# Optimization experiments

Measured on AMD Instinct MI355X. Metric: run time of the kernel, lower is better.

The kernel has to match this reference:

```python
import jax, jax.numpy as jnp
import numpy as np


def setup_inputs() -> dict:
    key = jax.random.key(0)
    rain_hr = jax.random.normal(key, (16, 8, 1, 512, 512), dtype=jnp.float32)
    return {"rain_hr": rain_hr}


def reference(rain_hr):
    B, T, C, H, W = rain_hr.shape
    rain_mean = rain_hr.mean(axis=1)              # [B, C, H, W]

    fft = jnp.fft.fft2(rain_mean)                 # complex [B, C, H, W]
    power = jnp.abs(fft) ** 2                     # [B, C, H, W]

    # Integer radius map (torch: sqrt(...).long() truncates toward zero)
    ch, cw = H // 2, W // 2
    y = jnp.arange(H, dtype=jnp.float32) - ch
    x = jnp.arange(W, dtype=jnp.float32) - cw
    radius = jnp.sqrt(x[None, :] ** 2 + y[:, None] ** 2).astype(jnp.int32)  # [H, W]

    max_radius = min(H, W) // 2

    # power[..., mask].mean() == sum over (B, C, pixels at radius r) / (B*C*count_r)
    power_hw = power.sum(axis=(0, 1))             # [H, W]
    flat_r = radius.ravel()
    # out-of-range radii (>= max_radius) are dropped by segment_sum
    seg_sum = jax.ops.segment_sum(power_hw.ravel(), flat_r, num_segments=max_radius)
    counts = jax.ops.segment_sum(jnp.ones((H * W,), jnp.float32), flat_r, num_segments=max_radius)

    cnt = counts[1:]                               # radii 1 .. max_radius-1
    denom = jnp.maximum(cnt, 1.0) * (B * C)
    gen_spectrum = jnp.where(cnt > 0, seg_sum[1:] / denom, 0.0)

    k = jnp.arange(1, max_radius, dtype=jnp.float32)
    ref = k ** (-5.0 / 3.0)
    ref = ref / (ref.sum() + 1e-8)

    gen_norm = gen_spectrum / (gen_spectrum.sum() + 1e-8)
    loss = jnp.mean((gen_norm - ref) ** 2)
    return loss
```

## Files before the change

### kernel.cpp

```cpp
#include <hip/hip_runtime.h>
#include <math.h>

#define N 512
#define PLANE ((size_t)N * N)
#define NEG2PI (-6.28318530717958647692f)

__device__ inline void dft8(float (&xr)[8], float (&xi)[8]) {
    const float S = 0.70710678118654752440f;
    float t0r = xr[0] + xr[4], t0i = xi[0] + xi[4];
    float t4r = xr[0] - xr[4], t4i = xi[0] - xi[4];
    float t1r = xr[1] + xr[5], t1i = xi[1] + xi[5];
    float t5r = xr[1] - xr[5], t5i = xi[1] - xi[5];
    float t2r = xr[2] + xr[6], t2i = xi[2] + xi[6];
    float t6r = xr[2] - xr[6], t6i = xi[2] - xi[6];
    float t3r = xr[3] + xr[7], t3i = xi[3] + xi[7];
    float t7r = xr[3] - xr[7], t7i = xi[3] - xi[7];
    float o1r = S * (t5r + t5i), o1i = S * (t5i - t5r);
    float o2r = t6i,             o2i = -t6r;
    float o3r = S * (t7i - t7r), o3i = -S * (t7r + t7i);
    float p0r = t0r + t2r, p0i = t0i + t2i;
    float p1r = t1r + t3r, p1i = t1i + t3i;
    float q0r = t0r - t2r, q0i = t0i - t2i;
    float q1r = t1i - t3i, q1i = -(t1r - t3r);
    xr[0] = p0r + p1r; xi[0] = p0i + p1i;
    xr[4] = p0r - p1r; xi[4] = p0i - p1i;
    xr[2] = q0r + q1r; xi[2] = q0i + q1i;
    xr[6] = q0r - q1r; xi[6] = q0i - q1i;
    float r0r = t4r + o2r, r0i = t4i + o2i;
    float r1r = o1r + o3r, r1i = o1i + o3i;
    float u0r = t4r - o2r, u0i = t4i - o2i;
    float u1r = o1i - o3i, u1i = -(o1r - o3r);
    xr[1] = r0r + r1r; xi[1] = r0i + r1i;
    xr[5] = r0r - r1r; xi[5] = r0i - r1i;
    xr[3] = u0r + u1r; xi[3] = u0i + u1i;
    xr[7] = u0r - u1r; xi[7] = u0i - u1i;
}

__device__ inline void twiddle_apply(float (&xr)[8], float (&xi)[8], float ang1) {
    float ts, tc;
    __sincosf(ang1, &ts, &tc);
    float wr = tc, wi = ts;
    #pragma unroll
    for (int k = 1; k < 8; ++k) {
        float nr = xr[k] * wr - xi[k] * wi;
        float ni = xr[k] * wi + xi[k] * wr;
        xr[k] = nr; xi[k] = ni;
        float w2r = wr * tc - wi * ts;
        float w2i = wr * ts + wi * tc;
        wr = w2r; wi = w2i;
    }
}

__device__ inline void fft512_wave(float (&xr)[8], float (&xi)[8],
                                   float* sre, float* sim, const int l) {
    dft8(xr, xi);
    twiddle_apply(xr, xi, (NEG2PI / 512.0f) * (float)l);
    const int w0 = l + (l >> 3);
    #pragma unroll
    for (int k = 0; k < 8; ++k) { sre[72 * k + w0] = xr[k]; sim[72 * k + w0] = xi[k]; }
    const int i2 = l & 7;
    const int rbase = 72 * (l >> 3) + i2;
    #pragma unroll
    for (int q = 0; q < 8; ++q) { xr[q] = sre[rbase + 9 * q]; xi[q] = sim[rbase + 9 * q]; }
    dft8(xr, xi);
    twiddle_apply(xr, xi, (NEG2PI / 64.0f) * (float)i2);
    #pragma unroll
    for (int k = 0; k < 8; ++k) { sre[rbase + 9 * k] = xr[k]; sim[rbase + 9 * k] = xi[k]; }
    const int r3 = 9 * l;
    #pragma unroll
    for (int q = 0; q < 8; ++q) { xr[q] = sre[r3 + q]; xi[q] = sim[r3 + q]; }
    dft8(xr, xi);
}

__global__ __launch_bounds__(256, 4) void kern_rowfft(const float* __restrict__ in,
                                                      float2* __restrict__ ws) {
    __shared__ float sRe[4][576];
    __shared__ float sIm[4][576];
    const int wv = threadIdx.x >> 6;
    const int l  = threadIdx.x & 63;
    const int y  = blockIdx.x * 4 + wv;
    const int j  = blockIdx.y;
    const float* baseA = in + ((size_t)j * 8) * PLANE + (size_t)y * N;
    const float* baseB = in + ((size_t)(j + 8) * 8) * PLANE + (size_t)y * N;
    float* re = sRe[wv];
    float* im = sIm[wv];
    #pragma unroll
    for (int c0 = 0; c0 < 2; ++c0) {
        const int c = l + 64 * c0;
        float4 sa = make_float4(0.f, 0.f, 0.f, 0.f);
        float4 sb = make_float4(0.f, 0.f, 0.f, 0.f);
        #pragma unroll
        for (int tt = 0; tt < 8; ++tt) {
            float4 a = *(const float4*)(baseA + tt * PLANE + 4 * c);
            float4 b = *(const float4*)(baseB + tt * PLANE + 4 * c);
            sa.x += a.x; sa.y += a.y; sa.z += a.z; sa.w += a.w;
            sb.x += b.x; sb.y += b.y; sb.z += b.z; sb.w += b.w;
        }
        const int i0 = 4 * c;
        const int p0 = i0 + (i0 >> 3);
        re[p0 + 0] = sa.x * 0.125f; re[p0 + 1] = sa.y * 0.125f;
        re[p0 + 2] = sa.z * 0.125f; re[p0 + 3] = sa.w * 0.125f;
        im[p0 + 0] = sb.x * 0.125f; im[p0 + 1] = sb.y * 0.125f;
        im[p0 + 2] = sb.z * 0.125f; im[p0 + 3] = sb.w * 0.125f;
    }
    float xr[8], xi[8];
    #pragma unroll
    for (int q = 0; q < 8; ++q) {
        const int p = l + (l >> 3) + 72 * q;
        xr[q] = re[p]; xi[q] = im[p];
    }
    fft512_wave(xr, xi, re, im, l);
    float2* wp = ws + ((size_t)j << 18) + ((size_t)y << 9);
    #pragma unroll
    for (int k = 0; k < 8; ++k) {
        wp[64 * k + 8 * (l & 7) + (l >> 3)] = make_float2(xr[k], xi[k]);
    }
}

__global__ __launch_bounds__(512, 4) void kern_colfft(const float2* __restrict__ ws,
                                                      float* __restrict__ gseg,
                                                      float* __restrict__ gcnt) {
    __shared__ float sA[8 * 576];
    __shared__ float sB[8 * 576];
    __shared__ float lseg[256];
    __shared__ float lcnt[256];
    const int w   = threadIdx.x >> 6;
    const int l   = threadIdx.x & 63;
    const int fx0 = blockIdx.x * 8;
    const int j   = blockIdx.y;
    if (threadIdx.x < 256) { lseg[threadIdx.x] = 0.f; lcnt[threadIdx.x] = 0.f; }
    const float2* base = ws + ((size_t)j << 18) + fx0;
    #pragma unroll
    for (int i = 0; i < 8; ++i) {
        const int y = (w << 6) + (i << 3) + (l >> 3);
        const int f = l & 7;
        float2 v = base[((size_t)y << 9) + f];
        sA[y * 9 + f] = v.x;
        sB[y * 9 + f] = v.y;
    }
    __syncthreads();
    float xr[8], xi[8];
    #pragma unroll
    for (int q = 0; q < 8; ++q) {
        const int y = l + (q << 6);
        xr[q] = sA[y * 9 + w];
        xi[q] = sB[y * 9 + w];
    }
    __syncthreads();
    fft512_wave(xr, xi, sA + w * 576, sB + w * 576, l);
    const int dx  = fx0 + w - 256;
    const int dx2 = dx * dx;
    #pragma unroll
    for (int k = 0; k < 8; ++k) {
        const int fy = 64 * k + 8 * (l & 7) + (l >> 3);
        const int dy = fy - 256;
        const int d2 = dx2 + dy * dy;
        int r = (int)sqrtf((float)d2);
        if ((r + 1) * (r + 1) <= d2) r++;
        else if (r * r > d2) r--;
        if (r >= 1 && r < 256) {
            atomicAdd(&lseg[r], xr[k] * xr[k] + xi[k] * xi[k]);
            if (j == 0) atomicAdd(&lcnt[r], 1.0f);
        }
    }
    __syncthreads();
    const int t = threadIdx.x;
    if (t < 256) {
        if (lseg[t] != 0.f) atomicAdd(&gseg[j * 256 + t], lseg[t]);
    } else if (j == 0) {
        if (lcnt[t - 256] != 0.f) atomicAdd(&gcnt[t - 256], lcnt[t - 256]);
    }
}

__global__ __launch_bounds__(256) void kern_loss(const float* __restrict__ gseg,
                                                 const float* __restrict__ gcnt,
                                                 float* __restrict__ out) {
    __shared__ float red[256];
    const int t = threadIdx.x;
    float gen = 0.f, refv = 0.f;
    if (t >= 1) {
        float s = 0.f;
        #pragma unroll
        for (int j = 0; j < 8; ++j) s += gseg[j * 256 + t];
        float c = gcnt[t];
        gen  = (c > 0.f) ? s / (fmaxf(c, 1.f) * 16.0f) : 0.f;
        refv = powf((float)t, -5.0f / 3.0f);
    }
    red[t] = gen; __syncthreads();
    for (int off = 128; off > 0; off >>= 1) {
        if (t < off) red[t] += red[t + off];
        __syncthreads();
    }
    const float sgen = red[0]; __syncthreads();
    red[t] = refv; __syncthreads();
    for (int off = 128; off > 0; off >>= 1) {
        if (t < off) red[t] += red[t + off];
        __syncthreads();
    }
    const float sref = red[0]; __syncthreads();
    const float gn = gen  / (sgen + 1e-8f);
    const float rn = refv / (sref + 1e-8f);
    red[t] = (gn - rn) * (gn - rn); __syncthreads();
    for (int off = 128; off > 0; off >>= 1) {
        if (t < off) red[t] += red[t + off];
        __syncthreads();
    }
    if (t == 0) out[0] = red[0] / 255.0f;
}

extern "C" void kernel_launch(void* const* d_in, const int* in_sizes, int n_in,
                              void* d_out, int out_size, void* d_ws, size_t ws_size,
                              hipStream_t stream) {
    const float* in = (const float*)d_in[0];
    float2* planes = (float2*)d_ws;
    float* bins = (float*)((char*)d_ws + (size_t)8 * N * N * sizeof(float2));
    float* gseg = bins;
    float* gcnt = bins + 8 * 256;
    hipMemsetAsync(bins, 0, (8 * 256 + 256) * sizeof(float), stream);
    kern_rowfft<<<dim3(128, 8), 256, 0, stream>>>(in, planes);
    kern_colfft<<<dim3(64, 8), 512, 0, stream>>>(planes, gseg, gcnt);
    kern_loss<<<1, 256, 0, stream>>>(gseg, gcnt, (float*)d_out);
}
```

Measured before the change: 216.8 us.

## Fold bin zeroing into row FFT, interleave block order, batch loads

```diff
diff --git a/kernel.cpp b/kernel.cpp
--- a/kernel.cpp
+++ b/kernel.cpp
@@ -37,8 +37,7 @@
 }
 
 __device__ inline void twiddle_apply(float (&xr)[8], float (&xi)[8], float ang1) {
-    float ts, tc;
-    __sincosf(ang1, &ts, &tc);
+    float ts = __sinf(ang1), tc = __cosf(ang1);
     float wr = tc, wi = ts;
     #pragma unroll
     for (int k = 1; k < 8; ++k) {
@@ -73,13 +72,20 @@
 }
 
 __global__ __launch_bounds__(256, 4) void kern_rowfft(const float* __restrict__ in,
-                                                      float2* __restrict__ ws) {
+                                                      float2* __restrict__ ws,
+                                                      float* __restrict__ bins) {
     __shared__ float sRe[4][576];
     __shared__ float sIm[4][576];
-    const int wv = threadIdx.x >> 6;
-    const int l  = threadIdx.x & 63;
-    const int y  = blockIdx.x * 4 + wv;
-    const int j  = blockIdx.y;
+    const int b   = blockIdx.x;
+    const int j   = b & 7;
+    const int sub = b >> 3;
+    const int wv  = threadIdx.x >> 6;
+    const int l   = threadIdx.x & 63;
+    const int y   = sub * 4 + wv;
+    if (b == 0) {
+        #pragma unroll
+        for (int i = 0; i < 9; ++i) bins[i * 256 + threadIdx.x] = 0.f;
+    }
     const float* baseA = in + ((size_t)j * 8) * PLANE + (size_t)y * N;
     const float* baseB = in + ((size_t)(j + 8) * 8) * PLANE + (size_t)y * N;
     float* re = sRe[wv];
@@ -87,15 +93,20 @@
     #pragma unroll
     for (int c0 = 0; c0 < 2; ++c0) {
         const int c = l + 64 * c0;
-        float4 sa = make_float4(0.f, 0.f, 0.f, 0.f);
-        float4 sb = make_float4(0.f, 0.f, 0.f, 0.f);
-        #pragma unroll
-        for (int tt = 0; tt < 8; ++tt) {
-            float4 a = *(const float4*)(baseA + tt * PLANE + 4 * c);
-            float4 b = *(const float4*)(baseB + tt * PLANE + 4 * c);
-            sa.x += a.x; sa.y += a.y; sa.z += a.z; sa.w += a.w;
-            sb.x += b.x; sb.y += b.y; sb.z += b.z; sb.w += b.w;
-        }
+        float4 va[8], vb[8];
+        #pragma unroll
+        for (int tt = 0; tt < 8; ++tt) va[tt] = *(const float4*)(baseA + tt * PLANE + 4 * c);
+        #pragma unroll
+        for (int tt = 0; tt < 8; ++tt) vb[tt] = *(const float4*)(baseB + tt * PLANE + 4 * c);
+        float4 sa, sb;
+        sa.x = ((va[0].x + va[1].x) + (va[2].x + va[3].x)) + ((va[4].x + va[5].x) + (va[6].x + va[7].x));
+        sa.y = ((va[0].y + va[1].y) + (va[2].y + va[3].y)) + ((va[4].y + va[5].y) + (va[6].y + va[7].y));
+        sa.z = ((va[0].z + va[1].z) + (va[2].z + va[3].z)) + ((va[4].z + va[5].z) + (va[6].z + va[7].z));
+        sa.w = ((va[0].w + va[1].w) + (va[2].w + va[3].w)) + ((va[4].w + va[5].w) + (va[6].w + va[7].w));
+        sb.x = ((vb[0].x + vb[1].x) + (vb[2].x + vb[3].x)) + ((vb[4].x + vb[5].x) + (vb[6].x + vb[7].x));
+        sb.y = ((vb[0].y + vb[1].y) + (vb[2].y + vb[3].y)) + ((vb[4].y + vb[5].y) + (vb[6].y + vb[7].y));
+        sb.z = ((vb[0].z + vb[1].z) + (vb[2].z + vb[3].z)) + ((vb[4].z + vb[5].z) + (vb[6].z + vb[7].z));
+        sb.w = ((vb[0].w + vb[1].w) + (vb[2].w + vb[3].w)) + ((vb[4].w + vb[5].w) + (vb[6].w + vb[7].w));
         const int i0 = 4 * c;
         const int p0 = i0 + (i0 >> 3);
         re[p0 + 0] = sa.x * 0.125f; re[p0 + 1] = sa.y * 0.125f;
@@ -124,11 +135,14 @@
     __shared__ float sB[8 * 576];
     __shared__ float lseg[256];
     __shared__ float lcnt[256];
-    const int w   = threadIdx.x >> 6;
-    const int l   = threadIdx.x & 63;
-    const int fx0 = blockIdx.x * 8;
-    const int j   = blockIdx.y;
-    if (threadIdx.x < 256) { lseg[threadIdx.x] = 0.f; lcnt[threadIdx.x] = 0.f; }
+    const int b   = blockIdx.x;
+    const int j   = b & 7;
+    const int sub = b >> 3;
+    const int fx0 = sub * 8;
+    const int t   = threadIdx.x;
+    const int w   = t >> 6;
+    const int l   = t & 63;
+    if (t < 256) { lseg[t] = 0.f; lcnt[t] = 0.f; }
     const float2* base = ws + ((size_t)j << 18) + fx0;
     #pragma unroll
     for (int i = 0; i < 8; ++i) {
@@ -164,7 +178,6 @@
         }
     }
     __syncthreads();
-    const int t = threadIdx.x;
     if (t < 256) {
         if (lseg[t] != 0.f) atomicAdd(&gseg[j * 256 + t], lseg[t]);
     } else if (j == 0) {
@@ -181,10 +194,10 @@
     if (t >= 1) {
         float s = 0.f;
         #pragma unroll
-        for (int j = 0; j < 8; ++j) s += gseg[j * 256 + t];
+        for (int jj = 0; jj < 8; ++jj) s += gseg[jj * 256 + t];
         float c = gcnt[t];
         gen  = (c > 0.f) ? s / (fmaxf(c, 1.f) * 16.0f) : 0.f;
-        refv = powf((float)t, -5.0f / 3.0f);
+        refv = exp2f(-1.66666666667f * log2f((float)t));
     }
     red[t] = gen; __syncthreads();
     for (int off = 128; off > 0; off >>= 1) {
@@ -216,8 +229,7 @@
     float* bins = (float*)((char*)d_ws + (size_t)8 * N * N * sizeof(float2));
     float* gseg = bins;
     float* gcnt = bins + 8 * 256;
-    hipMemsetAsync(bins, 0, (8 * 256 + 256) * sizeof(float), stream);
-    kern_rowfft<<<dim3(128, 8), 256, 0, stream>>>(in, planes);
-    kern_colfft<<<dim3(64, 8), 512, 0, stream>>>(planes, gseg, gcnt);
+    kern_rowfft<<<1024, 256, 0, stream>>>(in, planes, bins);
+    kern_colfft<<<512, 512, 0, stream>>>(planes, gseg, gcnt);
     kern_loss<<<1, 256, 0, stream>>>(gseg, gcnt, (float*)d_out);
 }
```

Result: no change. 216.6 us (-0.1%).
